# Kernel optimization log

Hardware: AMD Instinct MI355X
Metric: run time of the kernel (lower is better)

The kernel has to match this reference:

```python
import jax, jax.numpy as jnp
import numpy as np

TEMPERATURE = 8.0  # sqrt(d_head=64)

def setup_inputs() -> dict:
    key = jax.random.key(0)
    kq, kk, kv = jax.random.split(key, 3)
    shape = (2, 16, 2048, 64)  # [B, H, S, D]
    q = jax.random.normal(kq, shape, dtype=jnp.float32)
    k = jax.random.normal(kk, shape, dtype=jnp.float32)
    v = jax.random.normal(kv, shape, dtype=jnp.float32)
    return {"q": q, "k": k, "v": v}

def reference(q, k, v):
    # attn = softmax((q / temperature) @ k^T) ; dropout is identity in eval
    scores = jnp.einsum('bhqd,bhkd->bhqk', q / TEMPERATURE, k)  # [B,H,S,S]
    attn = jax.nn.softmax(scores, axis=-1)
    out = jnp.einsum('bhqk,bhkd->bhqd', attn, v)  # [B,H,S,D]
    return out
```

## Files before the change

kernel.cpp:

```cpp
#include <hip/hip_runtime.h>
#include <hip/hip_bf16.h>

typedef __bf16 bf16_t;
typedef bf16_t bf16x4 __attribute__((ext_vector_type(4)));
typedef bf16_t bf16x8 __attribute__((ext_vector_type(8)));
typedef float f32x4 __attribute__((ext_vector_type(4)));

#define S_LEN 2048
#define HD 64
#define NT 32
#define BHN 32
#define QSCALE 0.18033688f

__device__ __forceinline__ void gload16(const bf16_t* g, void* l) {
    __builtin_amdgcn_global_load_lds(
        (const __attribute__((address_space(1))) void*)g,
        (__attribute__((address_space(3))) void*)l, 16, 0, 0);
}

__global__ __launch_bounds__(256)
void prep_kv(const float* __restrict__ kg, const float* __restrict__ vg,
             bf16_t* __restrict__ kb, bf16_t* __restrict__ vtb) {
    __shared__ bf16_t Vl[64 * 68];
    const int tid = threadIdx.x;
    const int kt0 = blockIdx.x * 64;
    const int bh  = blockIdx.y;
    const size_t gbase = (size_t)bh * S_LEN * HD;
    #pragma unroll
    for (int j = 0; j < 4; ++j) {
        int idx = j * 256 + tid;
        int key = idx >> 4;
        int d0  = (idx & 15) * 4;
        const f32x4 k4 = *(const f32x4*)(kg + gbase + (size_t)(kt0 + key) * HD + d0);
        const f32x4 v4 = *(const f32x4*)(vg + gbase + (size_t)(kt0 + key) * HD + d0);
        bf16x4 kbv, vbv;
        #pragma unroll
        for (int e = 0; e < 4; ++e) { kbv[e] = (bf16_t)k4[e]; vbv[e] = (bf16_t)v4[e]; }
        *(bf16x4*)(kb + gbase + (size_t)(kt0 + key) * HD + d0) = kbv;
        *(bf16x4*)&Vl[key * 68 + d0] = vbv;
    }
    __syncthreads();
    const int d   = tid >> 2;
    const int q16 = tid & 3;
    const int kp  = q16 >> 1, h = q16 & 1;
    bf16_t* orow = vtb + (size_t)bh * HD * S_LEN + (size_t)d * S_LEN + kt0;
    #pragma unroll
    for (int gg = 0; gg < 4; ++gg) {
        bf16x4 o;
        #pragma unroll
        for (int r = 0; r < 4; ++r) o[r] = Vl[(q16 * 16 + gg * 4 + r) * 68 + d];
        *(bf16x4*)(orow + kp * 32 + gg * 8 + h * 4) = o;
    }
}

__global__ __launch_bounds__(256, 2)
void attn_fwd_bf16(const float* __restrict__ qg, const bf16_t* __restrict__ kb,
                   const bf16_t* __restrict__ vtb, float* __restrict__ og) {
    __shared__ __align__(16) char lds[32768];

    const int tid  = threadIdx.x;
    const int wave = tid >> 6;
    const int lane = tid & 63;
    const int g    = lane >> 4;
    const int ln   = lane & 15;

    const int fid  = blockIdx.x;
    const int bid2 = (fid & 7) * 64 + (fid >> 3);
    const int bh   = bid2 >> 4;
    const int qt   = bid2 & 15;
    const int qrow0 = qt * 128 + wave * 32;
    const size_t base = (size_t)bh * S_LEN * HD;

    bf16x8 qf[2][2];
    #pragma unroll
    for (int qg2 = 0; qg2 < 2; ++qg2) {
        const float* qp = qg + base + (size_t)(qrow0 + qg2 * 16 + ln) * HD;
        #pragma unroll
        for (int c = 0; c < 2; ++c)
            #pragma unroll
            for (int i = 0; i < 8; ++i)
                qf[qg2][c][i] = (bf16_t)(qp[c * 32 + g * 8 + i] * QSCALE);
    }

    bf16x8 ones;
    #pragma unroll
    for (int i = 0; i < 8; ++i) ones[i] = (bf16_t)1.0f;

    const int r0 = tid >> 3, s0 = tid & 7, r1 = r0 + 32;
    const bf16_t* kpl = kb + base;
    const bf16_t* vpl = vtb + base;
    const bf16_t* ksA = kpl + r0 * HD + (s0 ^ (r0 & 7)) * 8;
    const bf16_t* ksB = kpl + r1 * HD + (s0 ^ (r1 & 7)) * 8;
    const bf16_t* vsA = vpl + (size_t)r0 * S_LEN + (s0 ^ (r0 & 7)) * 8;
    const bf16_t* vsB = vpl + (size_t)r1 * S_LEN + (s0 ^ (r1 & 7)) * 8;
    char* ldb = lds + tid * 16;

#define STAGE_K(kt, b) do { \
        gload16(ksA + (size_t)(kt) * 4096, ldb + (b) * 8192); \
        gload16(ksB + (size_t)(kt) * 4096, ldb + (b) * 8192 + 4096); \
    } while (0)
#define STAGE_V(kt, b) do { \
        gload16(vsA + (kt) * 64, ldb + 16384 + (b) * 8192); \
        gload16(vsB + (kt) * 64, ldb + 16384 + (b) * 8192 + 4096); \
    } while (0)

    int kof[4][2], voff[4][2];
    #pragma unroll
    for (int kt2 = 0; kt2 < 4; ++kt2)
        #pragma unroll
        for (int c = 0; c < 2; ++c)
            kof[kt2][c] = (kt2 * 16 + ln) * 128 + (((c << 2) + g) ^ (ln & 7)) * 16;
    #pragma unroll
    for (int t = 0; t < 4; ++t)
        #pragma unroll
        for (int kp = 0; kp < 2; ++kp)
            voff[t][kp] = 16384 + (t * 16 + ln) * 128 + (((kp << 2) + g) ^ (ln & 7)) * 16;

    f32x4 acc[2][4];
    f32x4 accl[2];
    #pragma unroll
    for (int qg2 = 0; qg2 < 2; ++qg2) {
        accl[qg2] = f32x4{0.f, 0.f, 0.f, 0.f};
        #pragma unroll
        for (int t = 0; t < 4; ++t) acc[qg2][t] = f32x4{0.f, 0.f, 0.f, 0.f};
    }

    STAGE_K(0, 0);
    STAGE_V(0, 0);

    for (int kt = 0; kt < NT; ++kt) {
        asm volatile("s_waitcnt vmcnt(0)" ::: "memory");
        asm volatile("s_barrier" ::: "memory");
        if (kt + 1 < NT) {
            STAGE_K(kt + 1, (kt + 1) & 1);
            STAGE_V(kt + 1, (kt + 1) & 1);
        }
        const char* kbr = lds + (kt & 1) * 8192;
        const char* vbr = lds + (kt & 1) * 8192;

        f32x4 sv[4][2];
        __builtin_amdgcn_s_setprio(1);
        #pragma unroll
        for (int kt2 = 0; kt2 < 4; ++kt2) {
            const bf16x8 kf0 = *(const bf16x8*)(kbr + kof[kt2][0]);
            const bf16x8 kf1 = *(const bf16x8*)(kbr + kof[kt2][1]);
            #pragma unroll
            for (int qg2 = 0; qg2 < 2; ++qg2) {
                f32x4 s = f32x4{0.f, 0.f, 0.f, 0.f};
                s = __builtin_amdgcn_mfma_f32_16x16x32_bf16(kf0, qf[qg2][0], s, 0, 0, 0);
                s = __builtin_amdgcn_mfma_f32_16x16x32_bf16(kf1, qf[qg2][1], s, 0, 0, 0);
                sv[kt2][qg2] = s;
            }
        }
        __builtin_amdgcn_s_setprio(0);

        bf16x8 pa[2][2];
        #pragma unroll
        for (int qg2 = 0; qg2 < 2; ++qg2)
            #pragma unroll
            for (int kp = 0; kp < 2; ++kp)
                #pragma unroll
                for (int i = 0; i < 8; ++i)
                    pa[qg2][kp][i] = (bf16_t)__builtin_amdgcn_exp2f(sv[2 * kp + (i >> 2)][qg2][i & 3]);

        __builtin_amdgcn_s_setprio(1);
        #pragma unroll
        for (int qg2 = 0; qg2 < 2; ++qg2) {
            accl[qg2] = __builtin_amdgcn_mfma_f32_16x16x32_bf16(pa[qg2][0], ones, accl[qg2], 0, 0, 0);
            accl[qg2] = __builtin_amdgcn_mfma_f32_16x16x32_bf16(pa[qg2][1], ones, accl[qg2], 0, 0, 0);
        }
        #pragma unroll
        for (int t = 0; t < 4; ++t) {
            const bf16x8 vf0 = *(const bf16x8*)(vbr + voff[t][0]);
            const bf16x8 vf1 = *(const bf16x8*)(vbr + voff[t][1]);
            #pragma unroll
            for (int qg2 = 0; qg2 < 2; ++qg2) {
                acc[qg2][t] = __builtin_amdgcn_mfma_f32_16x16x32_bf16(pa[qg2][0], vf0, acc[qg2][t], 0, 0, 0);
                acc[qg2][t] = __builtin_amdgcn_mfma_f32_16x16x32_bf16(pa[qg2][1], vf1, acc[qg2][t], 0, 0, 0);
            }
        }
        __builtin_amdgcn_s_setprio(0);
    }
#undef STAGE_K
#undef STAGE_V

    #pragma unroll
    for (int qg2 = 0; qg2 < 2; ++qg2) {
        float* ob = og + base + (size_t)(qrow0 + qg2 * 16) * HD;
        float il[4];
        #pragma unroll
        for (int r = 0; r < 4; ++r) il[r] = 1.f / accl[qg2][r];
        #pragma unroll
        for (int t = 0; t < 4; ++t)
            #pragma unroll
            for (int r = 0; r < 4; ++r)
                ob[(size_t)(4 * g + r) * HD + t * 16 + ln] = acc[qg2][t][r] * il[r];
    }
}

#define LDP 72
__global__ __launch_bounds__(256, 2)
void attn_fwd_fallback(const float* __restrict__ qg, const float* __restrict__ kg,
                       const float* __restrict__ vg, float* __restrict__ og) {
    __shared__ __align__(16) bf16_t Kl[64 * LDP];
    __shared__ __align__(16) bf16_t Vt[HD * LDP];
    const int tid = threadIdx.x, wave = tid >> 6, lane = tid & 63;
    const int g = lane >> 4, ln = lane & 15;
    const int bh = blockIdx.y, qrow0 = blockIdx.x * 64 + wave * 16;
    const size_t base = (size_t)bh * S_LEN * HD;
    bf16x8 qf[2];
    {
        const float* qp = qg + base + (size_t)(qrow0 + ln) * HD;
        #pragma unroll
        for (int c = 0; c < 2; ++c)
            #pragma unroll
            for (int i = 0; i < 8; ++i) qf[c][i] = (bf16_t)(qp[c * 32 + g * 8 + i] * 0.125f);
    }
    f32x4 acc[4];
    #pragma unroll
    for (int t = 0; t < 4; ++t) acc[t] = f32x4{0.f, 0.f, 0.f, 0.f};
    float m_run = -3e38f, l_run = 0.f;
    const float* kbase = kg + base;
    const float* vbase = vg + base;
    const int vkb = (tid & 15) * 4, vdb = (tid >> 4) * 4;
    for (int kt = 0; kt < NT; ++kt) {
        __syncthreads();
        #pragma unroll
        for (int j = 0; j < 4; ++j) {
            int idx = j * 256 + tid, key = idx >> 4, d0 = (idx & 15) * 4;
            const f32x4 k4 = *(const f32x4*)(kbase + (size_t)(kt * 64 + key) * HD + d0);
            bf16x4 kbv;
            #pragma unroll
            for (int e = 0; e < 4; ++e) kbv[e] = (bf16_t)k4[e];
            *(bf16x4*)&Kl[key * LDP + d0] = kbv;
        }
        {
            f32x4 v4[4];
            #pragma unroll
            for (int e = 0; e < 4; ++e)
                v4[e] = *(const f32x4*)(vbase + (size_t)(kt * 64 + vkb + e) * HD + vdb);
            #pragma unroll
            for (int j = 0; j < 4; ++j) {
                bf16x4 vb;
                #pragma unroll
                for (int e = 0; e < 4; ++e) vb[e] = (bf16_t)v4[e][j];
                *(bf16x4*)&Vt[(vdb + j) * LDP + vkb] = vb;
            }
        }
        __syncthreads();
        float p[4][4];
        float mx = -3e38f;
        #pragma unroll
        for (int kt2 = 0; kt2 < 4; ++kt2) {
            f32x4 s = f32x4{0.f, 0.f, 0.f, 0.f};
            #pragma unroll
            for (int c = 0; c < 2; ++c) {
                const bf16x8 kf = *(const bf16x8*)&Kl[(kt2 * 16 + ln) * LDP + c * 32 + g * 8];
                s = __builtin_amdgcn_mfma_f32_16x16x32_bf16(kf, qf[c], s, 0, 0, 0);
            }
            #pragma unroll
            for (int r = 0; r < 4; ++r) { p[kt2][r] = s[r]; mx = fmaxf(mx, s[r]); }
        }
        mx = fmaxf(mx, __shfl_xor(mx, 16, 64));
        mx = fmaxf(mx, __shfl_xor(mx, 32, 64));
        const float mnew = fmaxf(m_run, mx);
        const float scale = __expf(m_run - mnew);
        m_run = mnew;
        float rs = 0.f;
        #pragma unroll
        for (int kt2 = 0; kt2 < 4; ++kt2)
            #pragma unroll
            for (int r = 0; r < 4; ++r) {
                const float e = __expf(p[kt2][r] - mnew);
                p[kt2][r] = e; rs += e;
            }
        rs += __shfl_xor(rs, 16, 64);
        rs += __shfl_xor(rs, 32, 64);
        l_run = l_run * scale + rs;
        float sc[4];
        #pragma unroll
        for (int r = 0; r < 4; ++r) sc[r] = __shfl(scale, 4 * g + r, 64);
        #pragma unroll
        for (int t = 0; t < 4; ++t)
            #pragma unroll
            for (int r = 0; r < 4; ++r) acc[t][r] *= sc[r];
        bf16x8 pa[2];
        #pragma unroll
        for (int kp = 0; kp < 2; ++kp)
            #pragma unroll
            for (int i = 0; i < 8; ++i) pa[kp][i] = (bf16_t)p[2 * kp + (i >> 2)][i & 3];
        #pragma unroll
        for (int t = 0; t < 4; ++t)
            #pragma unroll
            for (int kp = 0; kp < 2; ++kp) {
                const bf16_t* vrow = &Vt[(t * 16 + ln) * LDP + 32 * kp + 4 * g];
                const bf16x4 lo = *(const bf16x4*)(vrow);
                const bf16x4 hi = *(const bf16x4*)(vrow + 16);
                bf16x8 vf;
                #pragma unroll
                for (int e = 0; e < 4; ++e) { vf[e] = lo[e]; vf[4 + e] = hi[e]; }
                acc[t] = __builtin_amdgcn_mfma_f32_16x16x32_bf16(pa[kp], vf, acc[t], 0, 0, 0);
            }
    }
    const float invl = 1.f / l_run;
    float il[4];
    #pragma unroll
    for (int r = 0; r < 4; ++r) il[r] = __shfl(invl, 4 * g + r, 64);
    float* ob = og + base + (size_t)qrow0 * HD;
    #pragma unroll
    for (int t = 0; t < 4; ++t)
        #pragma unroll
        for (int r = 0; r < 4; ++r)
            ob[(size_t)(4 * g + r) * HD + t * 16 + ln] = acc[t][r] * il[r];
}

extern "C" void kernel_launch(void* const* d_in, const int* in_sizes, int n_in,
                              void* d_out, int out_size, void* d_ws, size_t ws_size,
                              hipStream_t stream) {
    const float* q = (const float*)d_in[0];
    const float* k = (const float*)d_in[1];
    const float* v = (const float*)d_in[2];
    float* out = (float*)d_out;
    const int bh = in_sizes[0] / (S_LEN * HD);
    const size_t plane = (size_t)bh * S_LEN * HD;
    const size_t need  = 2 * plane * sizeof(bf16_t);

    if (bh == BHN && ws_size >= need) {
        bf16_t* kb  = (bf16_t*)d_ws;
        bf16_t* vtb = kb + plane;
        prep_kv<<<dim3(NT, bh), 256, 0, stream>>>(k, v, kb, vtb);
        attn_fwd_bf16<<<dim3(bh * 16), 256, 0, stream>>>(q, kb, vtb, out);
    } else {
        attn_fwd_fallback<<<dim3(S_LEN / 64, bh), 256, 0, stream>>>(q, k, v, out);
    }
}
```

Measured before the change: 54.06 us.

## Triple-buffer K/V tiles in LDS with two-tile-ahead prefetch

```diff
diff --git a/kernel.cpp b/kernel.cpp
--- a/kernel.cpp
+++ b/kernel.cpp
@@ -56,7 +56,7 @@
 __global__ __launch_bounds__(256, 2)
 void attn_fwd_bf16(const float* __restrict__ qg, const bf16_t* __restrict__ kb,
                    const bf16_t* __restrict__ vtb, float* __restrict__ og) {
-    __shared__ __align__(16) char lds[32768];
+    __shared__ __align__(16) char lds[49152];
 
     const int tid  = threadIdx.x;
     const int wave = tid >> 6;
@@ -81,6 +81,7 @@
             for (int i = 0; i < 8; ++i)
                 qf[qg2][c][i] = (bf16_t)(qp[c * 32 + g * 8 + i] * QSCALE);
     }
+    asm volatile("s_waitcnt vmcnt(0)" ::: "memory");
 
     bf16x8 ones;
     #pragma unroll
@@ -95,13 +96,11 @@
     const bf16_t* vsB = vpl + (size_t)r1 * S_LEN + (s0 ^ (r1 & 7)) * 8;
     char* ldb = lds + tid * 16;
 
-#define STAGE_K(kt, b) do { \
+#define STAGE(kt, b) do { \
         gload16(ksA + (size_t)(kt) * 4096, ldb + (b) * 8192); \
         gload16(ksB + (size_t)(kt) * 4096, ldb + (b) * 8192 + 4096); \
-    } while (0)
-#define STAGE_V(kt, b) do { \
-        gload16(vsA + (kt) * 64, ldb + 16384 + (b) * 8192); \
-        gload16(vsB + (kt) * 64, ldb + 16384 + (b) * 8192 + 4096); \
+        gload16(vsA + (kt) * 64, ldb + 24576 + (b) * 8192); \
+        gload16(vsB + (kt) * 64, ldb + 24576 + (b) * 8192 + 4096); \
     } while (0)
 
     int kof[4][2], voff[4][2];
@@ -114,7 +113,7 @@
     for (int t = 0; t < 4; ++t)
         #pragma unroll
         for (int kp = 0; kp < 2; ++kp)
-            voff[t][kp] = 16384 + (t * 16 + ln) * 128 + (((kp << 2) + g) ^ (ln & 7)) * 16;
+            voff[t][kp] = 24576 + (t * 16 + ln) * 128 + (((kp << 2) + g) ^ (ln & 7)) * 16;
 
     f32x4 acc[2][4];
     f32x4 accl[2];
@@ -125,64 +124,61 @@
         for (int t = 0; t < 4; ++t) acc[qg2][t] = f32x4{0.f, 0.f, 0.f, 0.f};
     }
 
-    STAGE_K(0, 0);
-    STAGE_V(0, 0);
-
-    for (int kt = 0; kt < NT; ++kt) {
-        asm volatile("s_waitcnt vmcnt(0)" ::: "memory");
+#define COMPUTE(cbuf) do { \
+        const char* kbr = lds + (cbuf) * 8192; \
+        f32x4 sv[4][2]; \
+        __builtin_amdgcn_s_setprio(1); \
+        for (int kt2 = 0; kt2 < 4; ++kt2) { \
+            const bf16x8 kf0 = *(const bf16x8*)(kbr + kof[kt2][0]); \
+            const bf16x8 kf1 = *(const bf16x8*)(kbr + kof[kt2][1]); \
+            for (int qg2 = 0; qg2 < 2; ++qg2) { \
+                f32x4 s = f32x4{0.f, 0.f, 0.f, 0.f}; \
+                s = __builtin_amdgcn_mfma_f32_16x16x32_bf16(kf0, qf[qg2][0], s, 0, 0, 0); \
+                s = __builtin_amdgcn_mfma_f32_16x16x32_bf16(kf1, qf[qg2][1], s, 0, 0, 0); \
+                sv[kt2][qg2] = s; \
+            } \
+        } \
+        __builtin_amdgcn_s_setprio(0); \
+        bf16x8 pa[2][2]; \
+        for (int qg2 = 0; qg2 < 2; ++qg2) \
+            for (int kp = 0; kp < 2; ++kp) \
+                for (int i = 0; i < 8; ++i) \
+                    pa[qg2][kp][i] = (bf16_t)__builtin_amdgcn_exp2f(sv[2 * kp + (i >> 2)][qg2][i & 3]); \
+        __builtin_amdgcn_s_setprio(1); \
+        for (int qg2 = 0; qg2 < 2; ++qg2) { \
+            accl[qg2] = __builtin_amdgcn_mfma_f32_16x16x32_bf16(pa[qg2][0], ones, accl[qg2], 0, 0, 0); \
+            accl[qg2] = __builtin_amdgcn_mfma_f32_16x16x32_bf16(pa[qg2][1], ones, accl[qg2], 0, 0, 0); \
+        } \
+        for (int t = 0; t < 4; ++t) { \
+            const bf16x8 vf0 = *(const bf16x8*)(kbr + voff[t][0]); \
+            const bf16x8 vf1 = *(const bf16x8*)(kbr + voff[t][1]); \
+            for (int qg2 = 0; qg2 < 2; ++qg2) { \
+                acc[qg2][t] = __builtin_amdgcn_mfma_f32_16x16x32_bf16(pa[qg2][0], vf0, acc[qg2][t], 0, 0, 0); \
+                acc[qg2][t] = __builtin_amdgcn_mfma_f32_16x16x32_bf16(pa[qg2][1], vf1, acc[qg2][t], 0, 0, 0); \
+            } \
+        } \
+        __builtin_amdgcn_s_setprio(0); \
+    } while (0)
+
+    STAGE(0, 0);
+    STAGE(1, 1);
+
+    int cb = 0;
+    for (int kt = 0; kt < NT - 1; ++kt) {
+        asm volatile("s_waitcnt vmcnt(4)" ::: "memory");
         asm volatile("s_barrier" ::: "memory");
-        if (kt + 1 < NT) {
-            STAGE_K(kt + 1, (kt + 1) & 1);
-            STAGE_V(kt + 1, (kt + 1) & 1);
+        if (kt + 2 < NT) {
+            const int sb = (cb >= 1) ? cb - 1 : 2;
+            STAGE(kt + 2, sb);
         }
-        const char* kbr = lds + (kt & 1) * 8192;
-        const char* vbr = lds + (kt & 1) * 8192;
-
-        f32x4 sv[4][2];
-        __builtin_amdgcn_s_setprio(1);
-        #pragma unroll
-        for (int kt2 = 0; kt2 < 4; ++kt2) {
-            const bf16x8 kf0 = *(const bf16x8*)(kbr + kof[kt2][0]);
-            const bf16x8 kf1 = *(const bf16x8*)(kbr + kof[kt2][1]);
-            #pragma unroll
-            for (int qg2 = 0; qg2 < 2; ++qg2) {
-                f32x4 s = f32x4{0.f, 0.f, 0.f, 0.f};
-                s = __builtin_amdgcn_mfma_f32_16x16x32_bf16(kf0, qf[qg2][0], s, 0, 0, 0);
-                s = __builtin_amdgcn_mfma_f32_16x16x32_bf16(kf1, qf[qg2][1], s, 0, 0, 0);
-                sv[kt2][qg2] = s;
-            }
-        }
-        __builtin_amdgcn_s_setprio(0);
-
-        bf16x8 pa[2][2];
-        #pragma unroll
-        for (int qg2 = 0; qg2 < 2; ++qg2)
-            #pragma unroll
-            for (int kp = 0; kp < 2; ++kp)
-                #pragma unroll
-                for (int i = 0; i < 8; ++i)
-                    pa[qg2][kp][i] = (bf16_t)__builtin_amdgcn_exp2f(sv[2 * kp + (i >> 2)][qg2][i & 3]);
-
-        __builtin_amdgcn_s_setprio(1);
-        #pragma unroll
-        for (int qg2 = 0; qg2 < 2; ++qg2) {
-            accl[qg2] = __builtin_amdgcn_mfma_f32_16x16x32_bf16(pa[qg2][0], ones, accl[qg2], 0, 0, 0);
-            accl[qg2] = __builtin_amdgcn_mfma_f32_16x16x32_bf16(pa[qg2][1], ones, accl[qg2], 0, 0, 0);
-        }
-        #pragma unroll
-        for (int t = 0; t < 4; ++t) {
-            const bf16x8 vf0 = *(const bf16x8*)(vbr + voff[t][0]);
-            const bf16x8 vf1 = *(const bf16x8*)(vbr + voff[t][1]);
-            #pragma unroll
-            for (int qg2 = 0; qg2 < 2; ++qg2) {
-                acc[qg2][t] = __builtin_amdgcn_mfma_f32_16x16x32_bf16(pa[qg2][0], vf0, acc[qg2][t], 0, 0, 0);
-                acc[qg2][t] = __builtin_amdgcn_mfma_f32_16x16x32_bf16(pa[qg2][1], vf1, acc[qg2][t], 0, 0, 0);
-            }
-        }
-        __builtin_amdgcn_s_setprio(0);
-    }
-#undef STAGE_K
-#undef STAGE_V
+        COMPUTE(cb);
+        cb = (cb == 2) ? 0 : cb + 1;
+    }
+    asm volatile("s_waitcnt vmcnt(0)" ::: "memory");
+    asm volatile("s_barrier" ::: "memory");
+    COMPUTE(cb);
+#undef COMPUTE
+#undef STAGE
 
     #pragma unroll
     for (int qg2 = 0; qg2 < 2; ++qg2) {
```

After: 54.33 us. No clear change (+0.5%).

## Switch attention MFMAs from 16x16x32 to 32x32x16 tiles with matching V layout

Applied to the files above, without the earlier changes.

```diff
diff --git a/kernel.cpp b/kernel.cpp
--- a/kernel.cpp
+++ b/kernel.cpp
@@ -5,6 +5,7 @@
 typedef bf16_t bf16x4 __attribute__((ext_vector_type(4)));
 typedef bf16_t bf16x8 __attribute__((ext_vector_type(8)));
 typedef float f32x4 __attribute__((ext_vector_type(4)));
+typedef float f32x16 __attribute__((ext_vector_type(16)));
 
 #define S_LEN 2048
 #define HD 64
@@ -41,15 +42,14 @@
     }
     __syncthreads();
     const int d   = tid >> 2;
-    const int q16 = tid & 3;
-    const int kp  = q16 >> 1, h = q16 & 1;
-    bf16_t* orow = vtb + (size_t)bh * HD * S_LEN + (size_t)d * S_LEN + kt0;
-    #pragma unroll
-    for (int gg = 0; gg < 4; ++gg) {
+    const int g16 = tid & 3;
+    bf16_t* orow = vtb + (size_t)bh * HD * S_LEN + (size_t)d * S_LEN + kt0 + g16 * 16;
+    #pragma unroll
+    for (int a = 0; a < 4; ++a) {
         bf16x4 o;
         #pragma unroll
-        for (int r = 0; r < 4; ++r) o[r] = Vl[(q16 * 16 + gg * 4 + r) * 68 + d];
-        *(bf16x4*)(orow + kp * 32 + gg * 8 + h * 4) = o;
+        for (int r2 = 0; r2 < 4; ++r2) o[r2] = Vl[(g16 * 16 + a * 4 + r2) * 68 + d];
+        *(bf16x4*)(orow + 8 * (a & 1) + 4 * (a >> 1)) = o;
     }
 }
 
@@ -61,8 +61,8 @@
     const int tid  = threadIdx.x;
     const int wave = tid >> 6;
     const int lane = tid & 63;
-    const int g    = lane >> 4;
-    const int ln   = lane & 15;
+    const int q31  = lane & 31;
+    const int h    = lane >> 5;
 
     const int fid  = blockIdx.x;
     const int bid2 = (fid & 7) * 64 + (fid >> 3);
@@ -71,16 +71,16 @@
     const int qrow0 = qt * 128 + wave * 32;
     const size_t base = (size_t)bh * S_LEN * HD;
 
-    bf16x8 qf[2][2];
-    #pragma unroll
-    for (int qg2 = 0; qg2 < 2; ++qg2) {
-        const float* qp = qg + base + (size_t)(qrow0 + qg2 * 16 + ln) * HD;
-        #pragma unroll
-        for (int c = 0; c < 2; ++c)
+    bf16x8 qf[4];
+    {
+        const float* qp = qg + base + (size_t)(qrow0 + q31) * HD;
+        #pragma unroll
+        for (int c = 0; c < 4; ++c)
             #pragma unroll
             for (int i = 0; i < 8; ++i)
-                qf[qg2][c][i] = (bf16_t)(qp[c * 32 + g * 8 + i] * QSCALE);
-    }
+                qf[c][i] = (bf16_t)(qp[c * 16 + h * 8 + i] * QSCALE);
+    }
+    asm volatile("s_waitcnt vmcnt(0)" ::: "memory");
 
     bf16x8 ones;
     #pragma unroll
@@ -95,106 +95,91 @@
     const bf16_t* vsB = vpl + (size_t)r1 * S_LEN + (s0 ^ (r1 & 7)) * 8;
     char* ldb = lds + tid * 16;
 
-#define STAGE_K(kt, b) do { \
+#define STAGE(kt, b) do { \
         gload16(ksA + (size_t)(kt) * 4096, ldb + (b) * 8192); \
         gload16(ksB + (size_t)(kt) * 4096, ldb + (b) * 8192 + 4096); \
-    } while (0)
-#define STAGE_V(kt, b) do { \
         gload16(vsA + (kt) * 64, ldb + 16384 + (b) * 8192); \
         gload16(vsB + (kt) * 64, ldb + 16384 + (b) * 8192 + 4096); \
     } while (0)
 
-    int kof[4][2], voff[4][2];
-    #pragma unroll
-    for (int kt2 = 0; kt2 < 4; ++kt2)
-        #pragma unroll
-        for (int c = 0; c < 2; ++c)
-            kof[kt2][c] = (kt2 * 16 + ln) * 128 + (((c << 2) + g) ^ (ln & 7)) * 16;
-    #pragma unroll
-    for (int t = 0; t < 4; ++t)
-        #pragma unroll
-        for (int kp = 0; kp < 2; ++kp)
-            voff[t][kp] = 16384 + (t * 16 + ln) * 128 + (((kp << 2) + g) ^ (ln & 7)) * 16;
-
-    f32x4 acc[2][4];
-    f32x4 accl[2];
-    #pragma unroll
-    for (int qg2 = 0; qg2 < 2; ++qg2) {
-        accl[qg2] = f32x4{0.f, 0.f, 0.f, 0.f};
-        #pragma unroll
-        for (int t = 0; t < 4; ++t) acc[qg2][t] = f32x4{0.f, 0.f, 0.f, 0.f};
-    }
-
-    STAGE_K(0, 0);
-    STAGE_V(0, 0);
+    int kof[2][4];
+    #pragma unroll
+    for (int rb = 0; rb < 2; ++rb)
+        #pragma unroll
+        for (int c = 0; c < 4; ++c)
+            kof[rb][c] = (rb * 32 + q31) * 128 + (((c << 1) + h) ^ (q31 & 7)) * 16;
+    int voff[2][4];
+    #pragma unroll
+    for (int db = 0; db < 2; ++db)
+        #pragma unroll
+        for (int bc = 0; bc < 4; ++bc)
+            voff[db][bc] = 16384 + (db * 32 + q31) * 128 + ((((bc >> 1) << 2) + ((bc & 1) << 1) + h) ^ (q31 & 7)) * 16;
+
+    f32x16 acc[2];
+    f32x16 accl;
+    #pragma unroll
+    for (int i = 0; i < 16; ++i) { acc[0][i] = 0.f; acc[1][i] = 0.f; accl[i] = 0.f; }
+
+    STAGE(0, 0);
 
     for (int kt = 0; kt < NT; ++kt) {
         asm volatile("s_waitcnt vmcnt(0)" ::: "memory");
         asm volatile("s_barrier" ::: "memory");
-        if (kt + 1 < NT) {
-            STAGE_K(kt + 1, (kt + 1) & 1);
-            STAGE_V(kt + 1, (kt + 1) & 1);
-        }
+        if (kt + 1 < NT) STAGE(kt + 1, (kt + 1) & 1);
         const char* kbr = lds + (kt & 1) * 8192;
         const char* vbr = lds + (kt & 1) * 8192;
 
-        f32x4 sv[4][2];
+        f32x16 sv[2];
         __builtin_amdgcn_s_setprio(1);
         #pragma unroll
-        for (int kt2 = 0; kt2 < 4; ++kt2) {
-            const bf16x8 kf0 = *(const bf16x8*)(kbr + kof[kt2][0]);
-            const bf16x8 kf1 = *(const bf16x8*)(kbr + kof[kt2][1]);
-            #pragma unroll
-            for (int qg2 = 0; qg2 < 2; ++qg2) {
-                f32x4 s = f32x4{0.f, 0.f, 0.f, 0.f};
-                s = __builtin_amdgcn_mfma_f32_16x16x32_bf16(kf0, qf[qg2][0], s, 0, 0, 0);
-                s = __builtin_amdgcn_mfma_f32_16x16x32_bf16(kf1, qf[qg2][1], s, 0, 0, 0);
-                sv[kt2][qg2] = s;
-            }
+        for (int rb = 0; rb < 2; ++rb) {
+            f32x16 s;
+            #pragma unroll
+            for (int i = 0; i < 16; ++i) s[i] = 0.f;
+            #pragma unroll
+            for (int c = 0; c < 4; ++c) {
+                const bf16x8 kf = *(const bf16x8*)(kbr + kof[rb][c]);
+                s = __builtin_amdgcn_mfma_f32_32x32x16_bf16(kf, qf[c], s, 0, 0, 0);
+            }
+            sv[rb] = s;
         }
         __builtin_amdgcn_s_setprio(0);
 
-        bf16x8 pa[2][2];
-        #pragma unroll
-        for (int qg2 = 0; qg2 < 2; ++qg2)
-            #pragma unroll
-            for (int kp = 0; kp < 2; ++kp)
+        bf16x8 pa[4];
+        #pragma unroll
+        for (int b = 0; b < 2; ++b)
+            #pragma unroll
+            for (int c2 = 0; c2 < 2; ++c2)
                 #pragma unroll
                 for (int i = 0; i < 8; ++i)
-                    pa[qg2][kp][i] = (bf16_t)__builtin_amdgcn_exp2f(sv[2 * kp + (i >> 2)][qg2][i & 3]);
+                    pa[b * 2 + c2][i] = (bf16_t)__builtin_amdgcn_exp2f(sv[b][8 * c2 + i]);
 
         __builtin_amdgcn_s_setprio(1);
         #pragma unroll
-        for (int qg2 = 0; qg2 < 2; ++qg2) {
-            accl[qg2] = __builtin_amdgcn_mfma_f32_16x16x32_bf16(pa[qg2][0], ones, accl[qg2], 0, 0, 0);
-            accl[qg2] = __builtin_amdgcn_mfma_f32_16x16x32_bf16(pa[qg2][1], ones, accl[qg2], 0, 0, 0);
-        }
-        #pragma unroll
-        for (int t = 0; t < 4; ++t) {
-            const bf16x8 vf0 = *(const bf16x8*)(vbr + voff[t][0]);
-            const bf16x8 vf1 = *(const bf16x8*)(vbr + voff[t][1]);
-            #pragma unroll
-            for (int qg2 = 0; qg2 < 2; ++qg2) {
-                acc[qg2][t] = __builtin_amdgcn_mfma_f32_16x16x32_bf16(pa[qg2][0], vf0, acc[qg2][t], 0, 0, 0);
-                acc[qg2][t] = __builtin_amdgcn_mfma_f32_16x16x32_bf16(pa[qg2][1], vf1, acc[qg2][t], 0, 0, 0);
-            }
-        }
+        for (int bc = 0; bc < 4; ++bc)
+            accl = __builtin_amdgcn_mfma_f32_32x32x16_bf16(pa[bc], ones, accl, 0, 0, 0);
+        #pragma unroll
+        for (int db = 0; db < 2; ++db)
+            #pragma unroll
+            for (int bc = 0; bc < 4; ++bc) {
+                const bf16x8 vf = *(const bf16x8*)(vbr + voff[db][bc]);
+                acc[db] = __builtin_amdgcn_mfma_f32_32x32x16_bf16(pa[bc], vf, acc[db], 0, 0, 0);
+            }
         __builtin_amdgcn_s_setprio(0);
     }
-#undef STAGE_K
-#undef STAGE_V
-
-    #pragma unroll
-    for (int qg2 = 0; qg2 < 2; ++qg2) {
-        float* ob = og + base + (size_t)(qrow0 + qg2 * 16) * HD;
-        float il[4];
-        #pragma unroll
-        for (int r = 0; r < 4; ++r) il[r] = 1.f / accl[qg2][r];
-        #pragma unroll
-        for (int t = 0; t < 4; ++t)
-            #pragma unroll
-            for (int r = 0; r < 4; ++r)
-                ob[(size_t)(4 * g + r) * HD + t * 16 + ln] = acc[qg2][t][r] * il[r];
+#undef STAGE
+
+    float il[16];
+    #pragma unroll
+    for (int r = 0; r < 16; ++r) il[r] = 1.f / accl[r];
+    #pragma unroll
+    for (int db = 0; db < 2; ++db) {
+        float* ob = og + base + (size_t)qrow0 * HD + db * 32 + q31;
+        #pragma unroll
+        for (int r = 0; r < 16; ++r) {
+            const int qr = (r & 3) + 8 * (r >> 2) + 4 * h;
+            ob[(size_t)qr * HD] = acc[db][r] * il[r];
+        }
     }
 }
 
```

Measured after the change: 55.85 us. 1.03x slower.
